# Kernel tuning notes

Hardware: AMD Instinct MI355X
Metric: run time of the kernel (lower is better)

Reference implementation:

```python
import jax, jax.numpy as jnp
import numpy as np
from math import log

MODEL_DIM = 512
NUM_HEADS = 8
DIM_HEAD = 64
INNER = NUM_HEADS * DIM_HEAD
B, L = 8, 1024
EPS = 1e-5


def setup_inputs() -> dict:
    key = jax.random.key(0)
    ks = jax.random.split(key, 9)
    x = jax.random.normal(ks[0], (B, L, MODEL_DIM), dtype=jnp.float32)
    gamma = jnp.ones((MODEL_DIM,), jnp.float32)
    beta = jnp.zeros((MODEL_DIM,), jnp.float32)
    w_qkv = jax.random.normal(ks[1], (3 * INNER, MODEL_DIM), jnp.float32) * (MODEL_DIM ** -0.5)
    b_qkv = jnp.zeros((3 * INNER,), jnp.float32)
    w_pos = jax.random.normal(ks[2], (INNER, MODEL_DIM), jnp.float32) * (MODEL_DIM ** -0.5)
    w_out = jax.random.normal(ks[3], (MODEL_DIM, INNER), jnp.float32) * (INNER ** -0.5)
    b_out = jnp.zeros((MODEL_DIM,), jnp.float32)
    # xavier_uniform for (num_heads, dim_head)
    bound = (6.0 / (NUM_HEADS + DIM_HEAD)) ** 0.5
    u_bias = jax.random.uniform(ks[4], (NUM_HEADS, DIM_HEAD), jnp.float32, -bound, bound)
    v_bias = jax.random.uniform(ks[5], (NUM_HEADS, DIM_HEAD), jnp.float32, -bound, bound)
    return {"x": x, "gamma": gamma, "beta": beta, "w_qkv": w_qkv, "b_qkv": b_qkv,
            "w_pos": w_pos, "w_out": w_out, "b_out": b_out, "u_bias": u_bias, "v_bias": v_bias}


def _rel_pos_emb(seq_len, d):
    # (L, D): (i - j) scaled by sinusoid frequencies, then cos on even cols, sin on odd cols
    rel = (jnp.arange(seq_len, dtype=jnp.float32)[:, None]
           - jnp.arange(d, dtype=jnp.float32)[None, :])
    freqs = jnp.exp(-jnp.arange(0, 2 * d, 2, dtype=jnp.float32) * (log(10000.0) / MODEL_DIM))
    angle = rel * freqs[None, :]
    even = (jnp.arange(d) % 2) == 0
    return jnp.where(even[None, :], jnp.cos(angle), jnp.sin(angle))  # (L, D)


def reference(x, gamma, beta, w_qkv, b_qkv, w_pos, w_out, b_out, u_bias, v_bias):
    b, l, d = x.shape
    h, dh = NUM_HEADS, DIM_HEAD
    # LayerNorm
    mu = jnp.mean(x, axis=-1, keepdims=True)
    var = jnp.mean(jnp.square(x - mu), axis=-1, keepdims=True)
    xn = (x - mu) * jax.lax.rsqrt(var + EPS) * gamma + beta
    # relative position embedding, identical per batch element
    pe = _rel_pos_emb(l, d)                      # (L, D)
    pos = (pe @ w_pos.T).reshape(l, h, dh)       # (L, H, Dh)
    pos = jnp.transpose(pos, (1, 0, 2))          # (H, L, Dh)
    # qkv
    qkv = xn @ w_qkv.T + b_qkv                   # (B, L, 3*inner)
    q, k, v = jnp.split(qkv, 3, axis=-1)
    def to_heads(t):
        return jnp.transpose(t.reshape(b, l, h, dh), (0, 2, 1, 3))  # (B,H,L,Dh)
    q, k, v = to_heads(q), to_heads(k), to_heads(v)
    scale = dh ** -0.5
    content = jnp.einsum('bhld,bhmd->bhlm', q + u_bias[None, :, None, :], k)
    pos_score = jnp.einsum('bhld,hmd->bhlm', q + v_bias[None, :, None, :], pos)
    attn = jax.nn.softmax((content + pos_score) * scale, axis=-1)
    out = jnp.einsum('bhlm,bhmd->bhld', attn, v)
    out = jnp.transpose(out, (0, 2, 1, 3)).reshape(b, l, h * dh)
    return out @ w_out.T + b_out  # dropout p=0.0 -> identity
```

## Files before the change

### kernel.cpp

```cpp
#include <hip/hip_runtime.h>
#include <math.h>

static constexpr int Bn = 8, Ln = 1024, Dm = 512, Hn = 8, DhN = 64;

typedef short bf16x8 __attribute__((ext_vector_type(8)));
typedef float f32x4 __attribute__((ext_vector_type(4)));
typedef _Float16 f16x4 __attribute__((ext_vector_type(4)));
typedef _Float16 f16x8 __attribute__((ext_vector_type(8)));
typedef unsigned int u32x4 __attribute__((ext_vector_type(4)));

#define QSCALE 0.1803368801111137f

static __device__ __forceinline__ unsigned short f2b(float f) {
  union { float f; unsigned int u; } x;
  x.f = f;
  unsigned int u = x.u;
  unsigned int r = (u + 0x7FFFu + ((u >> 16) & 1u)) >> 16;
  return (unsigned short)r;
}
static __device__ __forceinline__ float b2f(unsigned short u) {
  union { unsigned int u; float f; } x;
  x.u = ((unsigned int)u) << 16;
  return x.f;
}

#define GLDS16(g, l)                                                        \
  __builtin_amdgcn_global_load_lds((const __attribute__((address_space(1))) void*)(g), \
                                   (__attribute__((address_space(3))) void*)(l), 16, 0, 0)

__global__ __launch_bounds__(256) void prep1(const float* __restrict__ x,
                                             const float* __restrict__ gamma,
                                             const float* __restrict__ beta,
                                             unsigned short* __restrict__ xn,
                                             unsigned short* __restrict__ pe,
                                             const float* __restrict__ wq, unsigned short* __restrict__ wqb,
                                             const float* __restrict__ wp, unsigned short* __restrict__ wpb,
                                             const float* __restrict__ wo, unsigned short* __restrict__ wob) {
  int b = blockIdx.x;
  int t = threadIdx.x;
  if (b < 8192) {
    const float2 v = *(const float2*)(x + (size_t)b * Dm + t * 2);
    float s = v.x + v.y;
    float sq = v.x * v.x + v.y * v.y;
#pragma unroll
    for (int off = 32; off > 0; off >>= 1) {
      s += __shfl_down(s, off);
      sq += __shfl_down(sq, off);
    }
    __shared__ float red[8];
    int wave = t >> 6, lane = t & 63;
    if (lane == 0) { red[wave * 2] = s; red[wave * 2 + 1] = sq; }
    __syncthreads();
    float S = red[0] + red[2] + red[4] + red[6];
    float SQ = red[1] + red[3] + red[5] + red[7];
    float mu = S * (1.0f / Dm);
    float var = SQ * (1.0f / Dm) - mu * mu;
    float rstd = rsqrtf(var + 1e-5f);
    int c = t * 2;
    ushort2 o;
    o.x = f2b((v.x - mu) * rstd * gamma[c] + beta[c]);
    o.y = f2b((v.y - mu) * rstd * gamma[c + 1] + beta[c + 1]);
    *(ushort2*)(xn + (size_t)b * Dm + c) = o;
  } else if (b < 10240) {
    int idx = (b - 8192) * 256 + t;
    int l = idx >> 9, k = idx & 511;
    float freq = expf(-0.0359778921f * (float)k);
    float angle = (float)(l - k) * freq;
    pe[idx] = f2b((k & 1) ? sinf(angle) : cosf(angle));
  } else {
    int cb = b - 10240;
    const float* src;
    unsigned short* dst;
    int off;
    if (cb < 768) { src = wq; dst = wqb; off = cb; }
    else if (cb < 1024) { src = wp; dst = wpb; off = cb - 768; }
    else { src = wo; dst = wob; off = cb - 1024; }
    int i = off * 256 + t;
    float4 v = *(const float4*)(src + (size_t)i * 4);
    ushort4 o;
    o.x = f2b(v.x); o.y = f2b(v.y); o.z = f2b(v.z); o.w = f2b(v.w);
    *(ushort4*)(dst + (size_t)i * 4) = o;
  }
}

__global__ __launch_bounds__(256, 8) void gemm_mfma(const unsigned short* __restrict__ Ain,
                                                    const unsigned short* __restrict__ Bwin,
                                                    const float* __restrict__ biasin,
                                                    float* __restrict__ outfin,
                                                    unsigned short* __restrict__ oq,
                                                    unsigned short* __restrict__ ok,
                                                    unsigned short* __restrict__ ov,
                                                    const unsigned short* __restrict__ A2,
                                                    const unsigned short* __restrict__ B2,
                                                    float* __restrict__ outf2,
                                                    int K, int mode) {
  int by = blockIdx.y, bx = blockIdx.x;
  const unsigned short* A = Ain;
  const unsigned short* Bw = Bwin;
  const float* bias = biasin;
  float* outf = outfin;
  if (by >= 128) {
    if (bx >= 8) return;
    A = A2; Bw = B2; bias = nullptr; outf = outf2; mode = 1; by -= 128;
  }
  __shared__ alignas(16) unsigned short As[64 * 64];
  __shared__ alignas(16) unsigned short Bs[64 * 64];
  const int t = threadIdx.x;
  const int lane = t & 63, w = t >> 6;
  const int c = lane & 15, q8 = lane >> 4;
  const int wm = (w & 1) * 32, wn = (w >> 1) * 32;
  const int m0 = by * 64, n0 = bx * 64;

  f32x4 acc[2][2];
#pragma unroll
  for (int i = 0; i < 2; ++i)
#pragma unroll
    for (int j = 0; j < 2; ++j) acc[i][j] = (f32x4){0.f, 0.f, 0.f, 0.f};

  const int srow = lane >> 3;
  const int sgr = (lane & 7) ^ srow;

  for (int k0 = 0; k0 < K; k0 += 64) {
    __syncthreads();
#pragma unroll
    for (int j = 0; j < 2; ++j) {
      int r = j * 32 + w * 8 + srow;
      GLDS16(A + (size_t)(m0 + r) * K + k0 + sgr * 8, As + (j * 256 + w * 64 + lane) * 8);
      GLDS16(Bw + (size_t)(n0 + r) * K + k0 + sgr * 8, Bs + (j * 256 + w * 64 + lane) * 8);
    }
    __syncthreads();
#pragma unroll
    for (int kk = 0; kk < 2; ++kk) {
      bf16x8 a[2], b[2];
      const int q = kk * 4 + q8;
#pragma unroll
      for (int i = 0; i < 2; ++i) {
        int r = wm + i * 16 + c;
        a[i] = *(const bf16x8*)&As[(r * 8 + (q ^ (r & 7))) * 8];
      }
#pragma unroll
      for (int j = 0; j < 2; ++j) {
        int r = wn + j * 16 + c;
        b[j] = *(const bf16x8*)&Bs[(r * 8 + (q ^ (r & 7))) * 8];
      }
#pragma unroll
      for (int i = 0; i < 2; ++i)
#pragma unroll
        for (int j = 0; j < 2; ++j)
          acc[i][j] = __builtin_amdgcn_mfma_f32_16x16x32_bf16(a[i], b[j], acc[i][j], 0, 0, 0);
    }
  }
#pragma unroll
  for (int i = 0; i < 2; ++i) {
#pragma unroll
    for (int r = 0; r < 4; ++r) {
      int m = m0 + wm + i * 16 + q8 * 4 + r;
#pragma unroll
      for (int j = 0; j < 2; ++j) {
        int n = n0 + wn + j * 16 + c;
        float val = acc[i][j][r] + (bias ? bias[n] : 0.0f);
        if (mode == 0) {
          int part = n >> 9, h = (n >> 6) & 7, dh = n & 63;
          int bb = m >> 10, l = m & 1023;
          size_t idx = (size_t)((bb * 8 + h) * 1024 + l) * 64 + dh;
          if (part == 0) {
            oq[idx] = f2b(val * QSCALE);
          } else if (part == 1) {
            ok[idx] = f2b(val);
          } else {
            union { _Float16 h; unsigned short u; } cv;
            cv.h = (_Float16)val;
            ov[idx] = cv.u;
          }
        } else if (mode == 1) {
          int h = n >> 6, dh = n & 63;
          outf[(size_t)(h * 1024 + m) * 64 + dh] = val;
        } else {
          outf[(size_t)m * 512 + n] = val;
        }
      }
    }
  }
}

__global__ __launch_bounds__(256) void prep2(unsigned short* __restrict__ kbuf,
                                             const float* __restrict__ pos,
                                             const float* __restrict__ ub,
                                             const float* __restrict__ vbb,
                                             float* __restrict__ biasout,
                                             const unsigned short* __restrict__ v,
                                             unsigned short* __restrict__ vt) {
  int b = blockIdx.x;
  int t = threadIdx.x;
  if (b < 16384) {
    int wave = t >> 6, lane = t & 63;
    int g = b * 4 + wave;
    int h = (g >> 10) & 7;
    int m = g & 1023;
    float kv = b2f(kbuf[(size_t)g * 64 + lane]);
    float pv = pos[(size_t)(h * 1024 + m) * 64 + lane];
    float val = ub[h * 64 + lane] * kv + vbb[h * 64 + lane] * pv;
#pragma unroll
    for (int off = 32; off > 0; off >>= 1) val += __shfl_down(val, off);
    if (lane == 0) biasout[g] = val * QSCALE;
    kbuf[(size_t)g * 64 + lane] = f2b(kv + pv);
  } else {
    __shared__ unsigned short Ts[64 * 68];
    int bb = b - 16384;
    int bh = bb >> 4, lt = bb & 15;
    const unsigned short* vg = v + (size_t)bh * 65536 + lt * 4096;
#pragma unroll
    for (int s = 0; s < 4; ++s) {
      int idx = t + s * 256;
      int r = idx >> 4, c4 = (idx & 15) << 2;
      *(ushort4*)&Ts[r * 68 + c4] = *(const ushort4*)(vg + r * 64 + c4);
    }
    __syncthreads();
#pragma unroll
    for (int s = 0; s < 4; ++s) {
      int idx = t + s * 256;
      int d = idx >> 4, l4 = (idx & 15) << 2;
      ushort4 o;
      o.x = Ts[(l4 + 0) * 68 + d];
      o.y = Ts[(l4 + 1) * 68 + d];
      o.z = Ts[(l4 + 2) * 68 + d];
      o.w = Ts[(l4 + 3) * 68 + d];
      int pb = ((l4 >> 2) & 3) * 16 + ((l4 >> 4) & 3) * 4;
      *(ushort4*)(vt + (size_t)bh * 65536 + d * 1024 + lt * 64 + pb) = o;
    }
  }
}

__global__ __launch_bounds__(256, 2) void flash_mfma(const unsigned short* __restrict__ qbf,
                                                     const unsigned short* __restrict__ kbf,
                                                     const unsigned short* __restrict__ vt,
                                                     const float* __restrict__ bias,
                                                     unsigned short* __restrict__ attn_out) {
  __shared__ alignas(16) unsigned short Ks[2][64 * 64];
  __shared__ alignas(16) unsigned short Vs[2][64 * 64];
  __shared__ alignas(16) float Bls[1024];
  const int t = threadIdx.x;
  const int lane = t & 63, w = t >> 6;
  const int c = lane & 15, q8 = lane >> 4;
  const int cc7 = c & 7;
  const int bh = blockIdx.y, qt = blockIdx.x;
  const unsigned short* qg = qbf + (size_t)bh * 65536;
  const unsigned short* kg = kbf + (size_t)bh * 65536;
  const unsigned short* vg = vt + (size_t)bh * 65536;
  const float* bg = bias + (size_t)bh * 1024;

  GLDS16(bg + t * 4, Bls + t * 4);

  bf16x8 bq[2][2];
#pragma unroll
  for (int g = 0; g < 2; ++g) {
    int qlg = qt * 128 + g * 64 + w * 16 + c;
    bq[g][0] = *(const bf16x8*)(qg + (size_t)qlg * 64 + q8 * 8);
    bq[g][1] = *(const bf16x8*)(qg + (size_t)qlg * 64 + 32 + q8 * 8);
  }

  float m_st[2] = {-INFINITY, -INFINITY};
  float l_st[2] = {0.0f, 0.0f};
  f32x4 o[2][4];
#pragma unroll
  for (int g = 0; g < 2; ++g)
#pragma unroll
    for (int i = 0; i < 4; ++i) o[g][i] = (f32x4){0.f, 0.f, 0.f, 0.f};

  const int srow = lane >> 3;
  const int sgr = (lane & 7) ^ srow;
  const int r0 = w * 16 + srow;

  u32x4 pk[2][2], pv[2][2];
#pragma unroll
  for (int h = 0; h < 2; ++h)
#pragma unroll
    for (int j = 0; j < 2; ++j) {
      int r = r0 + j * 8;
      pk[h][j] = *(const u32x4*)(kg + (size_t)(h * 64 + r) * 64 + sgr * 8);
      pv[h][j] = *(const u32x4*)(vg + (size_t)r * 1024 + h * 64 + sgr * 8);
    }

  for (int it = 0; it < 8; ++it) {
    __syncthreads();
#pragma unroll
    for (int h = 0; h < 2; ++h)
#pragma unroll
      for (int j = 0; j < 2; ++j) {
        int r = r0 + j * 8;
        *(u32x4*)&Ks[h][(r * 8 + (lane & 7)) * 8] = pk[h][j];
        *(u32x4*)&Vs[h][(r * 8 + (lane & 7)) * 8] = pv[h][j];
      }
    __syncthreads();
    if (it < 7) {
#pragma unroll
      for (int h = 0; h < 2; ++h)
#pragma unroll
        for (int j = 0; j < 2; ++j) {
          int r = r0 + j * 8;
          pk[h][j] = *(const u32x4*)(kg + (size_t)((it + 1) * 128 + h * 64 + r) * 64 + sgr * 8);
          pv[h][j] = *(const u32x4*)(vg + (size_t)r * 1024 + (it + 1) * 128 + h * 64 + sgr * 8);
        }
    }

    f32x4 sc[2][2][4];
#pragma unroll
    for (int h = 0; h < 2; ++h) {
#pragma unroll
      for (int nt = 0; nt < 4; ++nt) {
        f32x4 ci = *(const f32x4*)&Bls[it * 128 + h * 64 + nt * 16 + q8 * 4];
        const int row = nt * 16 + c;
        bf16x8 ak0 = *(const bf16x8*)&Ks[h][(row * 8 + (q8 ^ cc7)) * 8];
        bf16x8 ak1 = *(const bf16x8*)&Ks[h][(row * 8 + ((q8 + 4) ^ cc7)) * 8];
#pragma unroll
        for (int g = 0; g < 2; ++g) {
          f32x4 z = __builtin_amdgcn_mfma_f32_16x16x32_bf16(ak0, bq[g][0], ci, 0, 0, 0);
          sc[g][h][nt] = __builtin_amdgcn_mfma_f32_16x16x32_bf16(ak1, bq[g][1], z, 0, 0, 0);
        }
      }
    }
    float mx[2];
#pragma unroll
    for (int g = 0; g < 2; ++g) {
      float m = sc[g][0][0][0];
#pragma unroll
      for (int h = 0; h < 2; ++h)
#pragma unroll
        for (int nt = 0; nt < 4; ++nt)
#pragma unroll
          for (int r = 0; r < 4; ++r) m = fmaxf(m, sc[g][h][nt][r]);
      mx[g] = m;
    }
    {
      float s0 = __shfl_xor(mx[0], 16);
      float s1 = __shfl_xor(mx[1], 16);
      mx[0] = fmaxf(mx[0], s0);
      mx[1] = fmaxf(mx[1], s1);
      s0 = __shfl_xor(mx[0], 32);
      s1 = __shfl_xor(mx[1], 32);
      mx[0] = fmaxf(mx[0], s0);
      mx[1] = fmaxf(mx[1], s1);
    }
    f16x4 pf[2][2][4];
#pragma unroll
    for (int g = 0; g < 2; ++g) {
      float mn = fmaxf(m_st[g], mx[g]);
      float al = __builtin_amdgcn_exp2f(m_st[g] - mn);
      float su = 0.0f;
#pragma unroll
      for (int h = 0; h < 2; ++h)
#pragma unroll
        for (int nt = 0; nt < 4; ++nt)
#pragma unroll
          for (int r = 0; r < 4; ++r) {
            float p = __builtin_amdgcn_exp2f(sc[g][h][nt][r] - mn);
            su += p;
            pf[g][h][nt][r] = (_Float16)p;
          }
      l_st[g] = l_st[g] * al + su;
      m_st[g] = mn;
#pragma unroll
      for (int i = 0; i < 4; ++i) o[g][i] *= al;
    }
#pragma unroll
    for (int i = 0; i < 4; ++i) {
      const int row = i * 16 + c;
#pragma unroll
      for (int h = 0; h < 2; ++h) {
        f16x8 v01 = *(const f16x8*)&Vs[h][(row * 8 + ((2 * q8) ^ cc7)) * 8];
        f16x8 v23 = *(const f16x8*)&Vs[h][(row * 8 + ((2 * q8 + 1) ^ cc7)) * 8];
        f16x4 a0 = {v01[0], v01[1], v01[2], v01[3]};
        f16x4 a1 = {v01[4], v01[5], v01[6], v01[7]};
        f16x4 a2 = {v23[0], v23[1], v23[2], v23[3]};
        f16x4 a3 = {v23[4], v23[5], v23[6], v23[7]};
#pragma unroll
        for (int g = 0; g < 2; ++g) {
          o[g][i] = __builtin_amdgcn_mfma_f32_16x16x16f16(a0, pf[g][h][0], o[g][i], 0, 0, 0);
          o[g][i] = __builtin_amdgcn_mfma_f32_16x16x16f16(a1, pf[g][h][1], o[g][i], 0, 0, 0);
          o[g][i] = __builtin_amdgcn_mfma_f32_16x16x16f16(a2, pf[g][h][2], o[g][i], 0, 0, 0);
          o[g][i] = __builtin_amdgcn_mfma_f32_16x16x16f16(a3, pf[g][h][3], o[g][i], 0, 0, 0);
        }
      }
    }
  }
  float lt0 = l_st[0], lt1 = l_st[1];
  {
    float s0 = __shfl_xor(lt0, 16);
    float s1 = __shfl_xor(lt1, 16);
    lt0 += s0; lt1 += s1;
    s0 = __shfl_xor(lt0, 32);
    s1 = __shfl_xor(lt1, 32);
    lt0 += s0; lt1 += s1;
  }
  const int bidx = bh >> 3, h = bh & 7;
#pragma unroll
  for (int g = 0; g < 2; ++g) {
    int qlg = qt * 128 + g * 64 + w * 16 + c;
    float inv = 1.0f / (g == 0 ? lt0 : lt1);
    size_t base = (size_t)(bidx * 1024 + qlg) * 512 + h * 64;
#pragma unroll
    for (int i = 0; i < 4; ++i) {
      ushort4 ov4;
      ov4.x = f2b(o[g][i][0] * inv);
      ov4.y = f2b(o[g][i][1] * inv);
      ov4.z = f2b(o[g][i][2] * inv);
      ov4.w = f2b(o[g][i][3] * inv);
      *(ushort4*)(attn_out + base + i * 16 + q8 * 4) = ov4;
    }
  }
}

extern "C" void kernel_launch(void* const* d_in, const int* in_sizes, int n_in,
                              void* d_out, int out_size, void* d_ws, size_t ws_size,
                              hipStream_t stream) {
  const float* x      = (const float*)d_in[0];
  const float* gamma  = (const float*)d_in[1];
  const float* beta   = (const float*)d_in[2];
  const float* w_qkv  = (const float*)d_in[3];
  const float* b_qkv  = (const float*)d_in[4];
  const float* w_pos  = (const float*)d_in[5];
  const float* w_out  = (const float*)d_in[6];
  const float* b_out  = (const float*)d_in[7];
  const float* u_bias = (const float*)d_in[8];
  const float* v_bias = (const float*)d_in[9];
  float* out = (float*)d_out;

  unsigned short* wsu = (unsigned short*)d_ws;
  unsigned short* xnb   = wsu;
  unsigned short* peb   = wsu + 4194304;
  unsigned short* wqkvb = wsu + 4718592;
  unsigned short* wposb = wsu + 5505024;
  unsigned short* woutb = wsu + 5767168;
  unsigned short* qbf   = wsu + 6291456;
  unsigned short* kbf   = wsu + 10485760;
  unsigned short* vbf   = wsu + 14680064;
  unsigned short* vtb   = wsu + 18874368;
  unsigned short* attnb = wsu + 23068672;
  float* posb  = (float*)(wsu + 27262976);
  float* biasb = (float*)(wsu + 28311552);

  prep1<<<11520, 256, 0, stream>>>(x, gamma, beta, xnb, peb,
                                   w_qkv, wqkvb, w_pos, wposb, w_out, woutb);
  gemm_mfma<<<dim3(24, 144), 256, 0, stream>>>(xnb, wqkvb, b_qkv, nullptr, qbf, kbf, vbf,
                                               peb, wposb, posb, 512, 0);
  prep2<<<17408, 256, 0, stream>>>(kbf, posb, u_bias, v_bias, biasb, vbf, vtb);
  flash_mfma<<<dim3(8, 64), 256, 0, stream>>>(qbf, kbf, vtb, biasb, attnb);
  gemm_mfma<<<dim3(8, 128), 256, 0, stream>>>(attnb, woutb, b_out, out, nullptr, nullptr, nullptr,
                                              nullptr, nullptr, nullptr, 512, 2);
}
```

Baseline: 175.7 us.

## Fold pos GEMM into prep and fuse K+pos, bias and V transpose into QKV epilogue

The positional-embedding GEMM now runs inside prep1, which generates the sinusoid tile on the fly and converts w_pos to bf16 as it loads, also producing the v_bias·pos row sums. The QKV GEMM epilogue now adds pos to K, computes the u_bias·k dot product with a wave reduction to build the score bias, and writes V directly in the transposed, permuted layout. This removes the prep2 kernel launch, the pe and wpos bf16 buffers, and the extra reads and writes of K and V. In exchange the prep kernel carries heavier MFMA blocks that compute sin and cos, the GEMM epilogue has scattered V-transpose stores, and its occupancy hint drops from 8 to 6.

```diff
diff --git a/kernel.cpp b/kernel.cpp
--- a/kernel.cpp
+++ b/kernel.cpp
@@ -18,11 +18,6 @@
   unsigned int r = (u + 0x7FFFu + ((u >> 16) & 1u)) >> 16;
   return (unsigned short)r;
 }
-static __device__ __forceinline__ float b2f(unsigned short u) {
-  union { unsigned int u; float f; } x;
-  x.u = ((unsigned int)u) << 16;
-  return x.f;
-}
 
 #define GLDS16(g, l)                                                        \
   __builtin_amdgcn_global_load_lds((const __attribute__((address_space(1))) void*)(g), \
@@ -32,10 +27,16 @@
                                              const float* __restrict__ gamma,
                                              const float* __restrict__ beta,
                                              unsigned short* __restrict__ xn,
-                                             unsigned short* __restrict__ pe,
                                              const float* __restrict__ wq, unsigned short* __restrict__ wqb,
-                                             const float* __restrict__ wp, unsigned short* __restrict__ wpb,
-                                             const float* __restrict__ wo, unsigned short* __restrict__ wob) {
+                                             const float* __restrict__ wo, unsigned short* __restrict__ wob,
+                                             const float* __restrict__ wpos,
+                                             const float* __restrict__ vbias,
+                                             float* __restrict__ posb,
+                                             float* __restrict__ biasp) {
+  __shared__ float red[8];
+  __shared__ alignas(16) unsigned short Ap[4096];
+  __shared__ alignas(16) unsigned short Bp[4096];
+  __shared__ float Bred[4][32];
   int b = blockIdx.x;
   int t = threadIdx.x;
   if (b < 8192) {
@@ -47,7 +48,6 @@
       s += __shfl_down(s, off);
       sq += __shfl_down(sq, off);
     }
-    __shared__ float red[8];
     int wave = t >> 6, lane = t & 63;
     if (lane == 0) { red[wave * 2] = s; red[wave * 2 + 1] = sq; }
     __syncthreads();
@@ -61,50 +61,141 @@
     o.x = f2b((v.x - mu) * rstd * gamma[c] + beta[c]);
     o.y = f2b((v.y - mu) * rstd * gamma[c + 1] + beta[c + 1]);
     *(ushort2*)(xn + (size_t)b * Dm + c) = o;
-  } else if (b < 10240) {
-    int idx = (b - 8192) * 256 + t;
-    int l = idx >> 9, k = idx & 511;
-    float freq = expf(-0.0359778921f * (float)k);
-    float angle = (float)(l - k) * freq;
-    pe[idx] = f2b((k & 1) ? sinf(angle) : cosf(angle));
-  } else {
-    int cb = b - 10240;
+  } else if (b < 9216) {
     const float* src;
     unsigned short* dst;
     int off;
-    if (cb < 768) { src = wq; dst = wqb; off = cb; }
-    else if (cb < 1024) { src = wp; dst = wpb; off = cb - 768; }
-    else { src = wo; dst = wob; off = cb - 1024; }
+    if (b < 8960) { src = wq; dst = wqb; off = b - 8192; }
+    else { src = wo; dst = wob; off = b - 8960; }
     int i = off * 256 + t;
     float4 v = *(const float4*)(src + (size_t)i * 4);
     ushort4 o;
     o.x = f2b(v.x); o.y = f2b(v.y); o.z = f2b(v.z); o.w = f2b(v.w);
     *(ushort4*)(dst + (size_t)i * 4) = o;
+  } else {
+    int pb = b - 9216;
+    int by = pb >> 3, bx = pb & 7;
+    const int lane = t & 63, w = t >> 6;
+    const int c = lane & 15, q8 = lane >> 4;
+    const int wm = (w & 1) * 32, wn = (w >> 1) * 32;
+    const int m0 = by * 64, n0 = bx * 64;
+    f32x4 acc[2][2];
+#pragma unroll
+    for (int i = 0; i < 2; ++i)
+#pragma unroll
+      for (int j = 0; j < 2; ++j) acc[i][j] = (f32x4){0.f, 0.f, 0.f, 0.f};
+    const int srow = lane >> 3;
+    const int sgr = (lane & 7) ^ srow;
+    for (int k0 = 0; k0 < 512; k0 += 64) {
+      __syncthreads();
+#pragma unroll
+      for (int j = 0; j < 2; ++j) {
+        int r = j * 32 + w * 8 + srow;
+        int l = m0 + r;
+        int kbase = k0 + sgr * 8;
+        const float* wr = wpos + (size_t)(n0 + r) * 512 + kbase;
+        float4 b0 = *(const float4*)wr;
+        float4 b1 = *(const float4*)(wr + 4);
+        u32x4 bw;
+        bw[0] = (unsigned)f2b(b0.x) | ((unsigned)f2b(b0.y) << 16);
+        bw[1] = (unsigned)f2b(b0.z) | ((unsigned)f2b(b0.w) << 16);
+        bw[2] = (unsigned)f2b(b1.x) | ((unsigned)f2b(b1.y) << 16);
+        bw[3] = (unsigned)f2b(b1.z) | ((unsigned)f2b(b1.w) << 16);
+        u32x4 aw;
+#pragma unroll
+        for (int e = 0; e < 4; ++e) {
+          int k1 = kbase + e * 2;
+          float f1 = __expf(-0.0359778921f * (float)k1);
+          float f2_ = __expf(-0.0359778921f * (float)(k1 + 1));
+          float v1 = cosf((float)(l - k1) * f1);
+          float v2 = sinf((float)(l - k1 - 1) * f2_);
+          aw[e] = (unsigned)f2b(v1) | ((unsigned)f2b(v2) << 16);
+        }
+        *(u32x4*)&Ap[(j * 256 + w * 64 + lane) * 8] = aw;
+        *(u32x4*)&Bp[(j * 256 + w * 64 + lane) * 8] = bw;
+      }
+      __syncthreads();
+#pragma unroll
+      for (int kk = 0; kk < 2; ++kk) {
+        bf16x8 a[2], bb_[2];
+        const int q = kk * 4 + q8;
+#pragma unroll
+        for (int i = 0; i < 2; ++i) {
+          int rr = wm + i * 16 + c;
+          a[i] = *(const bf16x8*)&Ap[(rr * 8 + (q ^ (rr & 7))) * 8];
+        }
+#pragma unroll
+        for (int j = 0; j < 2; ++j) {
+          int rr = wn + j * 16 + c;
+          bb_[j] = *(const bf16x8*)&Bp[(rr * 8 + (q ^ (rr & 7))) * 8];
+        }
+#pragma unroll
+        for (int i = 0; i < 2; ++i)
+#pragma unroll
+          for (int j = 0; j < 2; ++j)
+            acc[i][j] = __builtin_amdgcn_mfma_f32_16x16x32_bf16(a[i], bb_[j], acc[i][j], 0, 0, 0);
+      }
+    }
+    float part[2][4];
+#pragma unroll
+    for (int i = 0; i < 2; ++i)
+#pragma unroll
+      for (int r = 0; r < 4; ++r) part[i][r] = 0.0f;
+#pragma unroll
+    for (int i = 0; i < 2; ++i) {
+#pragma unroll
+      for (int r = 0; r < 4; ++r) {
+        int m = m0 + wm + i * 16 + q8 * 4 + r;
+#pragma unroll
+        for (int j = 0; j < 2; ++j) {
+          int n = n0 + wn + j * 16 + c;
+          float val = acc[i][j][r];
+          posb[(size_t)((bx << 10) + m) * 64 + (n & 63)] = val;
+          part[i][r] += vbias[n] * val;
+        }
+      }
+    }
+#pragma unroll
+    for (int i = 0; i < 2; ++i)
+#pragma unroll
+      for (int r = 0; r < 4; ++r) {
+        float v = part[i][r];
+        v += __shfl_xor(v, 1);
+        v += __shfl_xor(v, 2);
+        v += __shfl_xor(v, 4);
+        v += __shfl_xor(v, 8);
+        part[i][r] = v;
+      }
+    if (c == 0) {
+#pragma unroll
+      for (int i = 0; i < 2; ++i)
+#pragma unroll
+        for (int r = 0; r < 4; ++r) Bred[w][i * 16 + q8 * 4 + r] = part[i][r];
+    }
+    __syncthreads();
+    if (t < 64) {
+      float s = (t < 32) ? (Bred[0][t] + Bred[2][t]) : (Bred[1][t - 32] + Bred[3][t - 32]);
+      biasp[(bx << 10) + m0 + t] = s * QSCALE;
+    }
   }
 }
 
-__global__ __launch_bounds__(256, 8) void gemm_mfma(const unsigned short* __restrict__ Ain,
-                                                    const unsigned short* __restrict__ Bwin,
-                                                    const float* __restrict__ biasin,
-                                                    float* __restrict__ outfin,
+__global__ __launch_bounds__(256, 6) void gemm_mfma(const unsigned short* __restrict__ A,
+                                                    const unsigned short* __restrict__ Bw,
+                                                    const float* __restrict__ bias,
+                                                    float* __restrict__ outf,
                                                     unsigned short* __restrict__ oq,
-                                                    unsigned short* __restrict__ ok,
-                                                    unsigned short* __restrict__ ov,
-                                                    const unsigned short* __restrict__ A2,
-                                                    const unsigned short* __restrict__ B2,
-                                                    float* __restrict__ outf2,
+                                                    unsigned short* __restrict__ kp,
+                                                    unsigned short* __restrict__ vt,
+                                                    const float* __restrict__ posb,
+                                                    const float* __restrict__ biasp,
+                                                    float* __restrict__ biasb,
+                                                    const float* __restrict__ ubias,
                                                     int K, int mode) {
-  int by = blockIdx.y, bx = blockIdx.x;
-  const unsigned short* A = Ain;
-  const unsigned short* Bw = Bwin;
-  const float* bias = biasin;
-  float* outf = outfin;
-  if (by >= 128) {
-    if (bx >= 8) return;
-    A = A2; Bw = B2; bias = nullptr; outf = outf2; mode = 1; by -= 128;
-  }
   __shared__ alignas(16) unsigned short As[64 * 64];
   __shared__ alignas(16) unsigned short Bs[64 * 64];
+  __shared__ float Bred[4][32];
+  int by = blockIdx.y, bx = blockIdx.x;
   const int t = threadIdx.x;
   const int lane = t & 63, w = t >> 6;
   const int c = lane & 15, q8 = lane >> 4;
@@ -150,6 +241,12 @@
           acc[i][j] = __builtin_amdgcn_mfma_f32_16x16x32_bf16(a[i], b[j], acc[i][j], 0, 0, 0);
     }
   }
+  const bool isK = (mode == 0) && (bx >= 8) && (bx < 16);
+  float uk[2][4];
+#pragma unroll
+  for (int i = 0; i < 2; ++i)
+#pragma unroll
+    for (int r = 0; r < 4; ++r) uk[i][r] = 0.0f;
 #pragma unroll
   for (int i = 0; i < 2; ++i) {
 #pragma unroll
@@ -166,67 +263,47 @@
           if (part == 0) {
             oq[idx] = f2b(val * QSCALE);
           } else if (part == 1) {
-            ok[idx] = f2b(val);
+            float pv = posb[(size_t)((h << 10) + l) * 64 + dh];
+            kp[idx] = f2b(val + pv);
+            uk[i][r] += ubias[h * 64 + dh] * val;
           } else {
-            union { _Float16 h; unsigned short u; } cv;
-            cv.h = (_Float16)val;
-            ov[idx] = cv.u;
+            int lb = l & 63;
+            int perm = ((lb >> 2) & 3) * 16 + ((lb >> 4) & 3) * 4 + (lb & 3);
+            union { _Float16 hf; unsigned short u; } cv;
+            cv.hf = (_Float16)val;
+            vt[(size_t)(bb * 8 + h) * 65536 + (size_t)dh * 1024 + (l & 960) + perm] = cv.u;
           }
-        } else if (mode == 1) {
-          int h = n >> 6, dh = n & 63;
-          outf[(size_t)(h * 1024 + m) * 64 + dh] = val;
         } else {
           outf[(size_t)m * 512 + n] = val;
         }
       }
     }
   }
-}
-
-__global__ __launch_bounds__(256) void prep2(unsigned short* __restrict__ kbuf,
-                                             const float* __restrict__ pos,
-                                             const float* __restrict__ ub,
-                                             const float* __restrict__ vbb,
-                                             float* __restrict__ biasout,
-                                             const unsigned short* __restrict__ v,
-                                             unsigned short* __restrict__ vt) {
-  int b = blockIdx.x;
-  int t = threadIdx.x;
-  if (b < 16384) {
-    int wave = t >> 6, lane = t & 63;
-    int g = b * 4 + wave;
-    int h = (g >> 10) & 7;
-    int m = g & 1023;
-    float kv = b2f(kbuf[(size_t)g * 64 + lane]);
-    float pv = pos[(size_t)(h * 1024 + m) * 64 + lane];
-    float val = ub[h * 64 + lane] * kv + vbb[h * 64 + lane] * pv;
-#pragma unroll
-    for (int off = 32; off > 0; off >>= 1) val += __shfl_down(val, off);
-    if (lane == 0) biasout[g] = val * QSCALE;
-    kbuf[(size_t)g * 64 + lane] = f2b(kv + pv);
-  } else {
-    __shared__ unsigned short Ts[64 * 68];
-    int bb = b - 16384;
-    int bh = bb >> 4, lt = bb & 15;
-    const unsigned short* vg = v + (size_t)bh * 65536 + lt * 4096;
-#pragma unroll
-    for (int s = 0; s < 4; ++s) {
-      int idx = t + s * 256;
-      int r = idx >> 4, c4 = (idx & 15) << 2;
-      *(ushort4*)&Ts[r * 68 + c4] = *(const ushort4*)(vg + r * 64 + c4);
-    }
-    __syncthreads();
-#pragma unroll
-    for (int s = 0; s < 4; ++s) {
-      int idx = t + s * 256;
-      int d = idx >> 4, l4 = (idx & 15) << 2;
-      ushort4 o;
-      o.x = Ts[(l4 + 0) * 68 + d];
-      o.y = Ts[(l4 + 1) * 68 + d];
-      o.z = Ts[(l4 + 2) * 68 + d];
-      o.w = Ts[(l4 + 3) * 68 + d];
-      int pb = ((l4 >> 2) & 3) * 16 + ((l4 >> 4) & 3) * 4;
-      *(ushort4*)(vt + (size_t)bh * 65536 + d * 1024 + lt * 64 + pb) = o;
+  if (isK) {
+#pragma unroll
+    for (int i = 0; i < 2; ++i)
+#pragma unroll
+      for (int r = 0; r < 4; ++r) {
+        float v = uk[i][r];
+        v += __shfl_xor(v, 1);
+        v += __shfl_xor(v, 2);
+        v += __shfl_xor(v, 4);
+        v += __shfl_xor(v, 8);
+        uk[i][r] = v;
+      }
+    if (c == 0) {
+#pragma unroll
+      for (int i = 0; i < 2; ++i)
+#pragma unroll
+        for (int r = 0; r < 4; ++r) Bred[w][i * 16 + q8 * 4 + r] = uk[i][r];
+    }
+    __syncthreads();
+    if (t < 64) {
+      float s = (t < 32) ? (Bred[0][t] + Bred[2][t]) : (Bred[1][t - 32] + Bred[3][t - 32]);
+      int m = m0 + t;
+      int bb = m >> 10, l = m & 1023;
+      int h = (n0 >> 6) & 7;
+      biasb[(size_t)(bb * 8 + h) * 1024 + l] = s * QSCALE + biasp[(h << 10) + l];
     }
   }
 }
@@ -427,24 +504,21 @@
 
   unsigned short* wsu = (unsigned short*)d_ws;
   unsigned short* xnb   = wsu;
-  unsigned short* peb   = wsu + 4194304;
-  unsigned short* wqkvb = wsu + 4718592;
-  unsigned short* wposb = wsu + 5505024;
-  unsigned short* woutb = wsu + 5767168;
-  unsigned short* qbf   = wsu + 6291456;
-  unsigned short* kbf   = wsu + 10485760;
-  unsigned short* vbf   = wsu + 14680064;
-  unsigned short* vtb   = wsu + 18874368;
-  unsigned short* attnb = wsu + 23068672;
-  float* posb  = (float*)(wsu + 27262976);
-  float* biasb = (float*)(wsu + 28311552);
-
-  prep1<<<11520, 256, 0, stream>>>(x, gamma, beta, xnb, peb,
-                                   w_qkv, wqkvb, w_pos, wposb, w_out, woutb);
-  gemm_mfma<<<dim3(24, 144), 256, 0, stream>>>(xnb, wqkvb, b_qkv, nullptr, qbf, kbf, vbf,
-                                               peb, wposb, posb, 512, 0);
-  prep2<<<17408, 256, 0, stream>>>(kbf, posb, u_bias, v_bias, biasb, vbf, vtb);
+  unsigned short* wqkvb = wsu + 4194304;
+  unsigned short* woutb = wsu + 4980736;
+  unsigned short* qbf   = wsu + 5242880;
+  unsigned short* kbf   = wsu + 9437184;
+  unsigned short* vtb   = wsu + 13631488;
+  unsigned short* attnb = wsu + 17825792;
+  float* posb  = (float*)(wsu + 22020096);
+  float* biasb = (float*)(wsu + 23068672);
+  float* biasp = (float*)(wsu + 23199744);
+
+  prep1<<<9344, 256, 0, stream>>>(x, gamma, beta, xnb, w_qkv, wqkvb, w_out, woutb,
+                                  w_pos, v_bias, posb, biasp);
+  gemm_mfma<<<dim3(24, 128), 256, 0, stream>>>(xnb, wqkvb, b_qkv, nullptr, qbf, kbf, vtb,
+                                               posb, biasp, biasb, u_bias, 512, 0);
   flash_mfma<<<dim3(8, 64), 256, 0, stream>>>(qbf, kbf, vtb, biasb, attnb);
   gemm_mfma<<<dim3(8, 128), 256, 0, stream>>>(attnb, woutb, b_out, out, nullptr, nullptr, nullptr,
-                                              nullptr, nullptr, nullptr, 512, 2);
+                                              nullptr, nullptr, nullptr, nullptr, 512, 2);
 }
```

Measured after the change: 197.0 us. 1.12x slower.
